# Performance work log

Hardware: AMD Instinct MI355X
Metric: run time of the kernel (lower is better)

The kernel has to match this reference:

```python
import jax, jax.numpy as jnp
import numpy as np

B, S, D, H = 4, 2048, 1024, 16
DK = D // H


def setup_inputs() -> dict:
    key = jax.random.key(0)
    ks = jax.random.split(key, 12)
    scale = 1.0 / np.sqrt(D)
    inp = {
        "query": jax.random.normal(ks[0], (B, S, D), jnp.float32),
        "key": jax.random.normal(ks[1], (B, S, D), jnp.float32),
        "value": jax.random.normal(ks[2], (B, S, D), jnp.float32),
        # lower-triangular causal mask broadcast over batch (1 = keep, 0 = masked)
        "mask": jnp.broadcast_to(jnp.tril(jnp.ones((S, S), jnp.bool_)), (B, S, S)),
        "wq": jax.random.normal(ks[3], (D, D), jnp.float32) * scale,
        "bq": jnp.zeros((D,), jnp.float32),
        "wk": jax.random.normal(ks[4], (D, D), jnp.float32) * scale,
        "bk": jnp.zeros((D,), jnp.float32),
        "wv": jax.random.normal(ks[5], (D, D), jnp.float32) * scale,
        "bv": jnp.zeros((D,), jnp.float32),
        "wo": jax.random.normal(ks[6], (D, D), jnp.float32) * scale,
        "bo": jnp.zeros((D,), jnp.float32),
    }
    return inp


def _split_heads(x):
    # [B, S, D] -> [B, H, S, DK]
    return x.reshape(B, S, H, DK).transpose(0, 2, 1, 3)


def reference(query, key, value, mask, wq, bq, wk, bk, wv, bv, wo, bo):
    # torch.nn.Linear: y = x @ W.T + b
    q = _split_heads(query @ wq.T + bq)
    k = _split_heads(key @ wk.T + bk)
    v = _split_heads(value @ wv.T + bv)

    scores = jnp.einsum("bhqd,bhkd->bhqk", q, k) / jnp.sqrt(jnp.float32(DK))
    # mask.unsqueeze(1): [B,1,S,S] broadcast over heads; masked_fill(mask==0, -1e9)
    scores = jnp.where(mask[:, None, :, :], scores, jnp.float32(-1e9))
    attn = jax.nn.softmax(scores, axis=-1)
    # dropout is identity in eval/reference mode

    ctx = jnp.einsum("bhqk,bhkd->bhqd", attn, v)  # [B,H,S,DK]
    ctx = ctx.transpose(0, 2, 1, 3).reshape(B, S, D)
    return ctx @ wo.T + bo
```

## Files before the change

kernel.cpp:

```cpp
#include <hip/hip_runtime.h>
#include <hip/hip_bf16.h>
#include <hip/hip_fp16.h>

#define B_  4
#define S_  2048
#define D_  1024
#define H_  16
#define DK_ 64

#define DT_F32  0
#define DT_BF16 1
#define DT_F16  2

typedef __bf16 bf16x8 __attribute__((ext_vector_type(8)));
typedef float  f32x4  __attribute__((ext_vector_type(4)));

__device__ __forceinline__ float bf2f(unsigned short u) {
    return __uint_as_float(((unsigned int)u) << 16);
}
__device__ __forceinline__ unsigned short f2bf(float f) {
    unsigned int u = __float_as_uint(f);
    return (unsigned short)((u + 0x7FFFu + ((u >> 16) & 1u)) >> 16);
}
__device__ __forceinline__ float h2f(unsigned short u) {
    union { __half h; unsigned short s; } cv; cv.s = u;
    return __half2float(cv.h);
}
__device__ __forceinline__ unsigned short f2h(float f) {
    union { __half h; unsigned short s; } cv; cv.h = __float2half(f);
    return cv.s;
}

__device__ __forceinline__ void gld_lds16(const void* g, void* l) {
    __builtin_amdgcn_global_load_lds(
        (const __attribute__((address_space(1))) void*)g,
        (__attribute__((address_space(3))) void*)l, 16, 0, 0);
}

template<int DT>
__device__ __forceinline__ float4 ld4(const void* base, size_t idx) {
    if constexpr (DT == DT_F32) {
        return *(const float4*)((const float*)base + idx);
    } else if constexpr (DT == DT_BF16) {
        ushort4 u = *(const ushort4*)((const unsigned short*)base + idx);
        return make_float4(bf2f(u.x), bf2f(u.y), bf2f(u.z), bf2f(u.w));
    } else {
        ushort4 u = *(const ushort4*)((const unsigned short*)base + idx);
        return make_float4(h2f(u.x), h2f(u.y), h2f(u.z), h2f(u.w));
    }
}
template<int DT>
__device__ __forceinline__ float ld1(const void* base, size_t idx) {
    if constexpr (DT == DT_F32)  return ((const float*)base)[idx];
    if constexpr (DT == DT_BF16) return bf2f(((const unsigned short*)base)[idx]);
    return h2f(((const unsigned short*)base)[idx]);
}

__global__ void detect_dtype(const unsigned short* __restrict__ q,
                             int* __restrict__ flag) {
    int c_bf = 0, c_hi = 0;
    for (int i = 0; i < 256; ++i) {
        const int e = (q[i] >> 7) & 0xFF;
        c_bf += (e >= 100 && e <= 140);
        c_hi += (e > 140);
    }
    *flag = (c_hi > 16) ? DT_F32 : ((c_bf >= 250) ? DT_BF16 : DT_F16);
}

__global__ __launch_bounds__(256) void convW(
    const float* __restrict__ wq, const float* __restrict__ wk,
    const float* __restrict__ wv,
    const float* __restrict__ bq, const float* __restrict__ bk,
    const float* __restrict__ bv,
    unsigned short* __restrict__ Wc, unsigned short* __restrict__ Bc,
    const int* __restrict__ flag)
{
    if (*flag != DT_F32) return;
    const size_t NW = (size_t)D_ * D_;
    const size_t i = (size_t)blockIdx.x * blockDim.x + threadIdx.x;
    if (i * 4 < NW) {
        const float* src[3] = {wq, wk, wv};
        #pragma unroll
        for (int j = 0; j < 3; ++j) {
            float4 f = ((const float4*)src[j])[i];
            ushort4 u; u.x = f2bf(f.x); u.y = f2bf(f.y); u.z = f2bf(f.z); u.w = f2bf(f.w);
            ((ushort4*)(Wc + j * NW))[i] = u;
        }
    }
    if (i * 4 < D_) {
        const float* src[3] = {bq, bk, bv};
        #pragma unroll
        for (int j = 0; j < 3; ++j) {
            float4 f = ((const float4*)src[j])[i];
            ushort4 u; u.x = f2bf(f.x); u.y = f2bf(f.y); u.z = f2bf(f.z); u.w = f2bf(f.w);
            ((ushort4*)(Bc + j * D_))[i] = u;
        }
    }
}

__global__ __launch_bounds__(256) void conv3(
    const float* __restrict__ a, unsigned short* __restrict__ da, size_t na,
    const float* __restrict__ w, unsigned short* __restrict__ dw, size_t nw,
    const float* __restrict__ b, unsigned short* __restrict__ db, size_t nb,
    const int* __restrict__ flag)
{
    if (*flag != DT_F32) return;
    const size_t i = (size_t)blockIdx.x * blockDim.x + threadIdx.x;
    if (i * 4 < na) {
        float4 f = ((const float4*)a)[i];
        ushort4 u; u.x = f2bf(f.x); u.y = f2bf(f.y); u.z = f2bf(f.z); u.w = f2bf(f.w);
        ((ushort4*)da)[i] = u;
    }
    if (i * 4 < nw) {
        float4 f = ((const float4*)w)[i];
        ushort4 u; u.x = f2bf(f.x); u.y = f2bf(f.y); u.z = f2bf(f.z); u.w = f2bf(f.w);
        ((ushort4*)dw)[i] = u;
    }
    if (i * 4 < nb) {
        float4 f = ((const float4*)b)[i];
        ushort4 u; u.x = f2bf(f.x); u.y = f2bf(f.y); u.z = f2bf(f.z); u.w = f2bf(f.w);
        ((ushort4*)db)[i] = u;
    }
}

template<bool AF32>
__device__ __forceinline__ void gemm_qkv_body(
    const void* __restrict__ X, const unsigned short* __restrict__ W,
    const unsigned short* __restrict__ Bi, unsigned short* __restrict__ Y,
    const int zmode)
{
    __shared__ __align__(16) unsigned short Ash[128 * 32];
    __shared__ __align__(16) unsigned short Bsh[128 * 32];
    const int tid  = threadIdx.x;
    const int wv   = tid >> 6, lane = tid & 63;
    const int quad = lane >> 4, l16 = lane & 15;
    const int wm   = wv >> 1,  wn   = wv & 1;
    const int m0   = blockIdx.y * 128, n0 = blockIdx.x * 128;

    f32x4 acc[4][4];
    #pragma unroll
    for (int nt = 0; nt < 4; ++nt) {
        const float bb = bf2f(Bi[n0 + wn * 64 + nt * 16 + l16]);
        #pragma unroll
        for (int mt = 0; mt < 4; ++mt) acc[mt][nt] = (f32x4){bb, bb, bb, bb};
    }

    const int srow = lane >> 2, sc4 = lane & 3;
    for (int kt = 0; kt < 32; ++kt) {
        #pragma unroll
        for (int ph = 0; ph < 2; ++ph) {
            const int i   = wv + ph * 4;
            const int row = i * 16 + srow;
            gld_lds16(W + (size_t)(n0 + row) * D_ + kt * 32 + sc4 * 8,
                      (char*)Bsh + i * 1024);
            unsigned short* dst = Ash + i * 512 + lane * 8;
            if constexpr (AF32) {
                const float* src = (const float*)X + (size_t)(m0 + row) * D_ + kt * 32 + sc4 * 8;
                const float4 a0 = ((const float4*)src)[0];
                const float4 a1 = ((const float4*)src)[1];
                bf16x8 vv;
                vv[0] = (__bf16)a0.x; vv[1] = (__bf16)a0.y;
                vv[2] = (__bf16)a0.z; vv[3] = (__bf16)a0.w;
                vv[4] = (__bf16)a1.x; vv[5] = (__bf16)a1.y;
                vv[6] = (__bf16)a1.z; vv[7] = (__bf16)a1.w;
                *(bf16x8*)dst = vv;
            } else {
                *(bf16x8*)dst = *(const bf16x8*)(
                    (const unsigned short*)X + (size_t)(m0 + row) * D_ + kt * 32 + sc4 * 8);
            }
        }
        __syncthreads();

        bf16x8 af[4], bfr[4];
        #pragma unroll
        for (int t = 0; t < 4; ++t) {
            af[t]  = *(const bf16x8*)(Ash + (wm * 64 + t * 16 + l16) * 32 + quad * 8);
            bfr[t] = *(const bf16x8*)(Bsh + (wn * 64 + t * 16 + l16) * 32 + quad * 8);
        }
        #pragma unroll
        for (int mt = 0; mt < 4; ++mt)
            #pragma unroll
            for (int nt = 0; nt < 4; ++nt)
                acc[mt][nt] = __builtin_amdgcn_mfma_f32_16x16x32_bf16(
                    af[mt], bfr[nt], acc[mt][nt], 0, 0, 0);
        __syncthreads();
    }

    #pragma unroll
    for (int mt = 0; mt < 4; ++mt) {
        const int mb = m0 + wm * 64 + mt * 16 + quad * 4;
        #pragma unroll
        for (int nt = 0; nt < 4; ++nt) {
            const int n = n0 + wn * 64 + nt * 16 + l16;
            const f32x4 a = acc[mt][nt];
            const int h = n >> 6, dk = n & 63;
            if (zmode != 2) {
                #pragma unroll
                for (int r = 0; r < 4; ++r) {
                    const int m = mb + r, b = m >> 11, s = m & (S_ - 1);
                    Y[(((size_t)(b * H_ + h) * S_ + s) << 6) + dk] = f2bf(a[r]);
                }
            } else {
                const int b = mb >> 11, s = mb & (S_ - 1);
                ushort4 u;
                u.x = f2bf(a[0]); u.y = f2bf(a[1]); u.z = f2bf(a[2]); u.w = f2bf(a[3]);
                *(ushort4*)(Y + (((size_t)(b * H_ + h) * DK_ + dk) << 11) + s) = u;
            }
        }
    }
}

__global__ __launch_bounds__(256) void gemm_qkv(
    const float* __restrict__ xq, const float* __restrict__ xk,
    const float* __restrict__ xv,
    const unsigned short* __restrict__ Wc,
    const unsigned short* __restrict__ wqb, const unsigned short* __restrict__ wkb,
    const unsigned short* __restrict__ wvb,
    const unsigned short* __restrict__ Bc,
    const unsigned short* __restrict__ bqb, const unsigned short* __restrict__ bkb,
    const unsigned short* __restrict__ bvb,
    unsigned short* __restrict__ Ybase,
    const int* __restrict__ flag)
{
    const int f = *flag;
    if (f == DT_F16) return;
    const int z = blockIdx.z;
    const size_t NE = (size_t)B_ * S_ * D_;
    const size_t NW = (size_t)D_ * D_;
    unsigned short* Y = Ybase + (size_t)z * NE;
    if (f == DT_F32) {
        const void* X = (z == 0) ? (const void*)xq : (z == 1) ? (const void*)xk : (const void*)xv;
        gemm_qkv_body<true>(X, Wc + (size_t)z * NW, Bc + (size_t)z * D_, Y, z);
    } else {
        const void* X = (z == 0) ? (const void*)xq : (z == 1) ? (const void*)xk : (const void*)xv;
        const unsigned short* W  = (z == 0) ? wqb : (z == 1) ? wkb : wvb;
        const unsigned short* Bi = (z == 0) ? bqb : (z == 1) ? bkb : bvb;
        gemm_qkv_body<false>(X, W, Bi, Y, z);
    }
}

template<int MODE>
__global__ __launch_bounds__(256) void gemm_mfma(
    const unsigned short* __restrict__ Xa, const unsigned short* __restrict__ Xb,
    const unsigned short* __restrict__ Wa, const unsigned short* __restrict__ Wb,
    const unsigned short* __restrict__ Ba, const unsigned short* __restrict__ Bb,
    void* __restrict__ Y,
    const int* __restrict__ flag)
{
    const int f = *flag;
    if (f == DT_F16) return;
    const unsigned short* X  = (f == DT_F32) ? Xa : Xb;
    const unsigned short* W  = (f == DT_F32) ? Wa : Wb;
    const unsigned short* Bi = (f == DT_F32) ? Ba : Bb;

    __shared__ __align__(16) unsigned short Ash[128 * 32];
    __shared__ __align__(16) unsigned short Bsh[128 * 32];
    const int tid  = threadIdx.x;
    const int wv   = tid >> 6, lane = tid & 63;
    const int quad = lane >> 4, l16 = lane & 15;
    const int wm   = wv >> 1,  wn   = wv & 1;
    const int m0   = blockIdx.y * 128, n0 = blockIdx.x * 128;

    f32x4 acc[4][4];
    #pragma unroll
    for (int nt = 0; nt < 4; ++nt) {
        const float bb = bf2f(Bi[n0 + wn * 64 + nt * 16 + l16]);
        #pragma unroll
        for (int mt = 0; mt < 4; ++mt) acc[mt][nt] = (f32x4){bb, bb, bb, bb};
    }

    const int srow = lane >> 2, sc4 = lane & 3;
    for (int kt = 0; kt < 32; ++kt) {
        #pragma unroll
        for (int ph = 0; ph < 2; ++ph) {
            const int i = wv + ph * 4;
            const int row = i * 16 + srow;
            gld_lds16(X + (size_t)(m0 + row) * D_ + kt * 32 + sc4 * 8,
                      (char*)Ash + i * 1024);
            gld_lds16(W + (size_t)(n0 + row) * D_ + kt * 32 + sc4 * 8,
                      (char*)Bsh + i * 1024);
        }
        __syncthreads();

        bf16x8 af[4], bfr[4];
        #pragma unroll
        for (int t = 0; t < 4; ++t) {
            af[t]  = *(const bf16x8*)(Ash + (wm * 64 + t * 16 + l16) * 32 + quad * 8);
            bfr[t] = *(const bf16x8*)(Bsh + (wn * 64 + t * 16 + l16) * 32 + quad * 8);
        }
        #pragma unroll
        for (int mt = 0; mt < 4; ++mt)
            #pragma unroll
            for (int nt = 0; nt < 4; ++nt)
                acc[mt][nt] = __builtin_amdgcn_mfma_f32_16x16x32_bf16(
                    af[mt], bfr[nt], acc[mt][nt], 0, 0, 0);
        __syncthreads();
    }

    #pragma unroll
    for (int mt = 0; mt < 4; ++mt) {
        const int mb = m0 + wm * 64 + mt * 16 + quad * 4;
        #pragma unroll
        for (int nt = 0; nt < 4; ++nt) {
            const int n = n0 + wn * 64 + nt * 16 + l16;
            const f32x4 a = acc[mt][nt];
            if constexpr (MODE == 0) {
                const int h = n >> 6, dk = n & 63;
                #pragma unroll
                for (int r = 0; r < 4; ++r) {
                    const int m = mb + r, b = m >> 11, s = m & (S_ - 1);
                    ((unsigned short*)Y)[(((size_t)(b * H_ + h) * S_ + s) << 6) + dk] = f2bf(a[r]);
                }
            } else if constexpr (MODE == 2) {
                const int h = n >> 6, dk = n & 63;
                const int b = mb >> 11, s = mb & (S_ - 1);
                ushort4 u;
                u.x = f2bf(a[0]); u.y = f2bf(a[1]); u.z = f2bf(a[2]); u.w = f2bf(a[3]);
                *(ushort4*)((unsigned short*)Y + (((size_t)(b * H_ + h) * DK_ + dk) << 11) + s) = u;
            } else {
                if (f == DT_F32) {
                    #pragma unroll
                    for (int r = 0; r < 4; ++r)
                        ((float*)Y)[(size_t)(mb + r) * D_ + n] = a[r];
                } else {
                    #pragma unroll
                    for (int r = 0; r < 4; ++r)
                        ((unsigned short*)Y)[(size_t)(mb + r) * D_ + n] = f2bf(a[r]);
                }
            }
        }
    }
}

__global__ __launch_bounds__(256) void attn_mfma(
    const unsigned short* __restrict__ Q,
    const unsigned short* __restrict__ K,
    const unsigned short* __restrict__ Vt,
    unsigned short* __restrict__ ctx)
{
    __shared__ __align__(16) unsigned short Ksh[2][2 * 64 * 32];
    __shared__ __align__(16) unsigned short Vsh[2][2 * 64 * 32];
    __shared__ __align__(16) __bf16         Psh[4][2 * 16 * 32];
    const int tid  = threadIdx.x;
    const int wv   = tid >> 6, lane = tid & 63;
    const int quad = lane >> 4, l16 = lane & 15;
    const int bx = blockIdx.x, bh = blockIdx.y;
    const unsigned short* Qb = Q  + (size_t)bh * S_ * DK_;
    const unsigned short* Kb = K  + (size_t)bh * S_ * DK_;
    const unsigned short* Vb = Vt + (size_t)bh * DK_ * S_;
    const int b = bh >> 4, h = bh & 15;
    const int srow = lane >> 2, sc4 = lane & 3;
    const int NT = S_ / 64;

    const float C1 = 0.125f * 1.44269504089f;
    const float C0 = -4.0f  * 1.44269504089f;

    auto stage = [&](int buf, int kt) {
        #pragma unroll
        for (int ph = 0; ph < 2; ++ph) {
            const int i  = wv + ph * 4;
            const int kk = i >> 2, r16 = i & 3;
            const int rr = r16 * 16 + srow;
            gld_lds16(Kb + (size_t)(kt * 64 + rr) * DK_ + kk * 32 + sc4 * 8,
                      (char*)(&Ksh[buf][0]) + i * 1024);
            gld_lds16(Vb + (size_t)rr * S_ + kt * 64 + kk * 32 + sc4 * 8,
                      (char*)(&Vsh[buf][0]) + i * 1024);
        }
    };

    #pragma unroll
    for (int seg = 0; seg < 2; ++seg) {
        const int qt = seg ? (NT - 1 - bx) : bx;
        const int q0 = qt * 64;

        const int qrow = q0 + wv * 16 + l16;
        bf16x8 qf0 = *(const bf16x8*)(Qb + (size_t)qrow * DK_ + quad * 8);
        bf16x8 qf1 = *(const bf16x8*)(Qb + (size_t)qrow * DK_ + 32 + quad * 8);

        f32x4 o[4];
        #pragma unroll
        for (int t = 0; t < 4; ++t) o[t] = (f32x4){0.f, 0.f, 0.f, 0.f};
        float lsum[4] = {0.f, 0.f, 0.f, 0.f};
        const int rowb = q0 + wv * 16 + quad * 4;

        stage(0, 0);

        for (int kt = 0; kt <= qt; ++kt) {
            const int cur = kt & 1;
            if (kt < qt) {
                stage(cur ^ 1, kt + 1);
                asm volatile("s_waitcnt vmcnt(4)" ::: "memory");
            } else {
                asm volatile("s_waitcnt vmcnt(0)" ::: "memory");
            }
            __builtin_amdgcn_s_barrier();
            asm volatile("" ::: "memory");

            const unsigned short* Kc = &Ksh[cur][0];
            const unsigned short* Vc = &Vsh[cur][0];

            f32x4 st[4];
            #pragma unroll
            for (int t = 0; t < 4; ++t) {
                bf16x8 k0 = *(const bf16x8*)(Kc + (t * 16 + l16) * 32 + quad * 8);
                bf16x8 k1 = *(const bf16x8*)(Kc + 2048 + (t * 16 + l16) * 32 + quad * 8);
                f32x4 z = (f32x4){0.f, 0.f, 0.f, 0.f};
                st[t] = __builtin_amdgcn_mfma_f32_16x16x32_bf16(qf0, k0, z, 0, 0, 0);
                st[t] = __builtin_amdgcn_mfma_f32_16x16x32_bf16(qf1, k1, st[t], 0, 0, 0);
            }

            float p[4][4];
            if (kt == qt) {
                #pragma unroll
                for (int t = 0; t < 4; ++t) {
                    const int col = kt * 64 + t * 16 + l16;
                    #pragma unroll
                    for (int r = 0; r < 4; ++r) {
                        float sv = fmaf(st[t][r], C1, C0);
                        if (col > rowb + r) sv = -1e9f;
                        p[t][r] = __builtin_amdgcn_exp2f(sv);
                        lsum[r] += p[t][r];
                    }
                }
            } else {
                #pragma unroll
                for (int t = 0; t < 4; ++t)
                    #pragma unroll
                    for (int r = 0; r < 4; ++r) {
                        p[t][r] = __builtin_amdgcn_exp2f(fmaf(st[t][r], C1, C0));
                        lsum[r] += p[t][r];
                    }
            }

            #pragma unroll
            for (int t = 0; t < 4; ++t) {
                const int col = t * 16 + l16;
                const int kk = col >> 5, c32 = col & 31, g = c32 >> 3;
                #pragma unroll
                for (int r = 0; r < 4; ++r) {
                    const int row = quad * 4 + r;
                    Psh[wv][kk * 512 + row * 32 + ((g ^ quad) * 8) + (c32 & 7)] =
                        (__bf16)p[t][r];
                }
            }

            bf16x8 pf[2];
            #pragma unroll
            for (int kk = 0; kk < 2; ++kk)
                pf[kk] = *(const bf16x8*)(&Psh[wv][kk * 512 + l16 * 32 + ((quad ^ (l16 >> 2)) * 8)]);
            #pragma unroll
            for (int t = 0; t < 4; ++t) {
                bf16x8 v0 = *(const bf16x8*)(Vc + (t * 16 + l16) * 32 + quad * 8);
                bf16x8 v1 = *(const bf16x8*)(Vc + 2048 + (t * 16 + l16) * 32 + quad * 8);
                o[t] = __builtin_amdgcn_mfma_f32_16x16x32_bf16(pf[0], v0, o[t], 0, 0, 0);
                o[t] = __builtin_amdgcn_mfma_f32_16x16x32_bf16(pf[1], v1, o[t], 0, 0, 0);
            }
            __syncthreads();
        }

        float li[4];
        #pragma unroll
        for (int r = 0; r < 4; ++r) {
            float l = lsum[r];
            l += __shfl_xor(l, 1, 64);
            l += __shfl_xor(l, 2, 64);
            l += __shfl_xor(l, 4, 64);
            l += __shfl_xor(l, 8, 64);
            li[r] = 1.0f / l;
        }
        #pragma unroll
        for (int t = 0; t < 4; ++t)
            #pragma unroll
            for (int r = 0; r < 4; ++r) {
                const int row = rowb + r;
                ctx[(size_t)(b * S_ + row) * D_ + h * DK_ + t * 16 + l16] =
                    f2bf(o[t][r] * li[r]);
            }
    }
}

template<int MODE, int DT>
__global__ __launch_bounds__(256) void gemm_xwT(
    const void* __restrict__ X,
    const void* __restrict__ W,
    const void* __restrict__ bias,
    void* __restrict__ Y,
    const int* __restrict__ flag)
{
    if (*flag != DT) return;
    constexpr int XDT = (MODE == 1) ? DT_BF16 : DT;

    __shared__ float As[16][65];
    __shared__ float Bs[16][65];
    const int tid = threadIdx.x;
    const int n0 = blockIdx.x * 64;
    const int m0 = blockIdx.y * 64;
    const int tx = tid & 15, ty = tid >> 4;
    const int lr = tid >> 2, lc = (tid & 3) << 2;

    float acc[4][4] = {};
    const size_t xbase = (size_t)(m0 + lr) * D_ + lc;
    const size_t wbase = (size_t)(n0 + lr) * D_ + lc;

    for (int k0 = 0; k0 < D_; k0 += 16) {
        const float4 a = ld4<XDT>(X, xbase + k0);
        const float4 b = ld4<DT >(W, wbase + k0);
        As[lc + 0][lr] = a.x; As[lc + 1][lr] = a.y;
        As[lc + 2][lr] = a.z; As[lc + 3][lr] = a.w;
        Bs[lc + 0][lr] = b.x; Bs[lc + 1][lr] = b.y;
        Bs[lc + 2][lr] = b.z; Bs[lc + 3][lr] = b.w;
        __syncthreads();
        #pragma unroll
        for (int k = 0; k < 16; ++k) {
            float av[4], bv[4];
            #pragma unroll
            for (int i = 0; i < 4; ++i) { av[i] = As[k][ty * 4 + i]; bv[i] = Bs[k][tx * 4 + i]; }
            #pragma unroll
            for (int i = 0; i < 4; ++i)
                #pragma unroll
                for (int j = 0; j < 4; ++j) acc[i][j] += av[i] * bv[j];
        }
        __syncthreads();
    }

    #pragma unroll
    for (int i = 0; i < 4; ++i) {
        const int m = m0 + ty * 4 + i;
        #pragma unroll
        for (int j = 0; j < 4; ++j) {
            const int n = n0 + tx * 4 + j;
            const float y = acc[i][j] + ld1<DT>(bias, n);
            if constexpr (MODE == 0) {
                const int b = m >> 11, s = m & (S_ - 1), h = n >> 6, dk = n & 63;
                ((unsigned short*)Y)[(((size_t)(b * H_ + h) * S_ + s) << 6) + dk] = f2bf(y);
            } else if constexpr (MODE == 2) {
                const int b = m >> 11, s = m & (S_ - 1), h = n >> 6, dk = n & 63;
                ((unsigned short*)Y)[(((size_t)(b * H_ + h) * DK_ + dk) << 11) + s] = f2bf(y);
            } else {
                const size_t oi = (size_t)m * D_ + n;
                if constexpr (DT == DT_F32)       ((float*)Y)[oi] = y;
                else if constexpr (DT == DT_BF16) ((unsigned short*)Y)[oi] = f2bf(y);
                else                              ((unsigned short*)Y)[oi] = f2h(y);
            }
        }
    }
}

__global__ void copy_out(const ulong2* __restrict__ src, ulong2* __restrict__ dst,
                         size_t out_size, const int* __restrict__ flag) {
    const size_t bytes  = out_size * ((*flag == DT_F32) ? 4u : 2u);
    const size_t chunks = bytes >> 4;
    const size_t i = (size_t)blockIdx.x * blockDim.x + threadIdx.x;
    if (i < chunks) dst[i] = src[i];
}

extern "C" void kernel_launch(void* const* d_in, const int* in_sizes, int n_in,
                              void* d_out, int out_size, void* d_ws, size_t ws_size,
                              hipStream_t stream) {
    const int wi = (n_in >= 12) ? 4 : 3;
    const void* q  = d_in[0];
    const void* k  = d_in[1];
    const void* v  = d_in[2];
    const void* wq = d_in[wi + 0];
    const void* bq = d_in[wi + 1];
    const void* wk = d_in[wi + 2];
    const void* bk = d_in[wi + 3];
    const void* wv = d_in[wi + 4];
    const void* bv = d_in[wi + 5];
    const void* wo = d_in[wi + 6];
    const void* bo = d_in[wi + 7];

    const size_t NE = (size_t)B_ * S_ * D_;
    const size_t NW = (size_t)D_ * D_;

    int* flag = (int*)d_ws;
    unsigned short* Qw = (unsigned short*)((char*)d_ws + 256);
    unsigned short* Kw = Qw + NE;
    unsigned short* Vw = Kw + NE;
    unsigned short* Cw = Vw + NE;

    const bool planA = ws_size >= 256 + 4 * NE * 2;

    unsigned short* xconv = (unsigned short*)d_out;
    unsigned short* Wc    = xconv + NE;
    unsigned short* Bc    = Wc + 4 * NW;

    unsigned short* ctx  = planA ? Cw : xconv;
    void*           yfin = planA ? d_out : (void*)Qw;
    unsigned short* WoC = planA ? Kw : (Wc + 3 * NW);
    unsigned short* BoC = planA ? (Kw + NW) : (Bc + 3 * D_);

    detect_dtype<<<1, 1, 0, stream>>>((const unsigned short*)q, flag);

    const dim3 gqkv(D_ / 128, (B_ * S_) / 128, 3);
    const dim3 gm(D_ / 128, (B_ * S_) / 128);
    const dim3 gs(D_ / 64,  (B_ * S_) / 64);
    const int  wgrid = (int)((NW / 4 + 255) / 256);

    convW<<<wgrid, 256, 0, stream>>>((const float*)wq, (const float*)wk,
                                     (const float*)wv,
                                     (const float*)bq, (const float*)bk,
                                     (const float*)bv,
                                     Wc, Bc, flag);

    gemm_qkv<<<gqkv, 256, 0, stream>>>(
        (const float*)q, (const float*)k, (const float*)v,
        Wc,
        (const unsigned short*)wq, (const unsigned short*)wk,
        (const unsigned short*)wv,
        Bc,
        (const unsigned short*)bq, (const unsigned short*)bk,
        (const unsigned short*)bv,
        Qw, flag);

    gemm_xwT<0, DT_F16><<<gs, 256, 0, stream>>>(q, wq, bq, Qw, flag);
    gemm_xwT<0, DT_F16><<<gs, 256, 0, stream>>>(k, wk, bk, Kw, flag);
    gemm_xwT<2, DT_F16><<<gs, 256, 0, stream>>>(v, wv, bv, Vw, flag);

    attn_mfma<<<dim3(S_ / 128, B_ * H_), 256, 0, stream>>>(Qw, Kw, Vw, ctx);

    conv3<<<wgrid, 256, 0, stream>>>((const float*)nullptr, (unsigned short*)nullptr, 0,
                                     (const float*)wo, WoC, NW,
                                     (const float*)bo, BoC, D_, flag);

    gemm_mfma<1><<<gm, 256, 0, stream>>>(ctx, ctx,
                                         WoC, (const unsigned short*)wo,
                                         BoC, (const unsigned short*)bo,
                                         yfin, flag);
    gemm_xwT<1, DT_F16><<<gs, 256, 0, stream>>>((const void*)ctx, wo, bo, yfin, flag);

    if (!planA) {
        const size_t maxChunks = ((size_t)out_size * 4) >> 4;
        copy_out<<<(int)((maxChunks + 255) / 256), 256, 0, stream>>>(
            (const ulong2*)yfin, (ulong2*)d_out, (size_t)out_size, flag);
    }
}
```

Measured before the change: 416.1 us.

## Double-buffer LDS in QKV and output GEMMs and remap block order

Double-buffers the shared-memory tiles of the QKV projection and output projection GEMMs. Each iteration prefetches the next K tile (register-staged for the fp32 A operand, direct global-to-LDS for the rest) while computing on the current one, with explicit waitcnt and barrier control in place of two __syncthreads per step. It also remaps the flat block index so blocks scheduled together are spread across row tiles, which could change cache reuse of X and W. The cost is twice the LDS, which may reduce occupancy, plus fragile hand-written vmcnt counts.

```diff
diff --git a/kernel.cpp b/kernel.cpp
--- a/kernel.cpp
+++ b/kernel.cpp
@@ -127,15 +127,15 @@
 __device__ __forceinline__ void gemm_qkv_body(
     const void* __restrict__ X, const unsigned short* __restrict__ W,
     const unsigned short* __restrict__ Bi, unsigned short* __restrict__ Y,
-    const int zmode)
+    const int zmode, const int m0, const int n0)
 {
-    __shared__ __align__(16) unsigned short Ash[128 * 32];
-    __shared__ __align__(16) unsigned short Bsh[128 * 32];
+    __shared__ __align__(16) unsigned short Ash[2][128 * 32];
+    __shared__ __align__(16) unsigned short Bsh[2][128 * 32];
     const int tid  = threadIdx.x;
     const int wv   = tid >> 6, lane = tid & 63;
     const int quad = lane >> 4, l16 = lane & 15;
     const int wm   = wv >> 1,  wn   = wv & 1;
-    const int m0   = blockIdx.y * 128, n0 = blockIdx.x * 128;
+    const int srow = lane >> 2, sc4 = lane & 3;
 
     f32x4 acc[4][4];
     #pragma unroll
@@ -145,37 +145,61 @@
         for (int mt = 0; mt < 4; ++mt) acc[mt][nt] = (f32x4){bb, bb, bb, bb};
     }
 
-    const int srow = lane >> 2, sc4 = lane & 3;
-    for (int kt = 0; kt < 32; ++kt) {
+    float4 ra00, ra01, ra10, ra11;
+    bf16x8 rb0, rb1;
+
+    auto aload = [&](int kt) {
+        #pragma unroll
+        for (int ph = 0; ph < 2; ++ph) {
+            const int i   = wv + ph * 4;
+            const int row = i * 16 + srow;
+            if constexpr (AF32) {
+                const float* src = (const float*)X + (size_t)(m0 + row) * D_ + kt * 32 + sc4 * 8;
+                float4 x0 = ((const float4*)src)[0];
+                float4 x1 = ((const float4*)src)[1];
+                if (ph == 0) { ra00 = x0; ra01 = x1; } else { ra10 = x0; ra11 = x1; }
+            } else {
+                const unsigned short* src =
+                    (const unsigned short*)X + (size_t)(m0 + row) * D_ + kt * 32 + sc4 * 8;
+                bf16x8 x = *(const bf16x8*)src;
+                if (ph == 0) rb0 = x; else rb1 = x;
+            }
+        }
+    };
+    auto awrite = [&](int buf) {
+        #pragma unroll
+        for (int ph = 0; ph < 2; ++ph) {
+            const int i = wv + ph * 4;
+            unsigned short* dst = &Ash[buf][0] + i * 512 + lane * 8;
+            if constexpr (AF32) {
+                const float4 x0 = ph ? ra10 : ra00;
+                const float4 x1 = ph ? ra11 : ra01;
+                bf16x8 vv;
+                vv[0] = (__bf16)x0.x; vv[1] = (__bf16)x0.y;
+                vv[2] = (__bf16)x0.z; vv[3] = (__bf16)x0.w;
+                vv[4] = (__bf16)x1.x; vv[5] = (__bf16)x1.y;
+                vv[6] = (__bf16)x1.z; vv[7] = (__bf16)x1.w;
+                *(bf16x8*)dst = vv;
+            } else {
+                *(bf16x8*)dst = ph ? rb1 : rb0;
+            }
+        }
+    };
+    auto stageB = [&](int buf, int kt) {
         #pragma unroll
         for (int ph = 0; ph < 2; ++ph) {
             const int i   = wv + ph * 4;
             const int row = i * 16 + srow;
             gld_lds16(W + (size_t)(n0 + row) * D_ + kt * 32 + sc4 * 8,
-                      (char*)Bsh + i * 1024);
-            unsigned short* dst = Ash + i * 512 + lane * 8;
-            if constexpr (AF32) {
-                const float* src = (const float*)X + (size_t)(m0 + row) * D_ + kt * 32 + sc4 * 8;
-                const float4 a0 = ((const float4*)src)[0];
-                const float4 a1 = ((const float4*)src)[1];
-                bf16x8 vv;
-                vv[0] = (__bf16)a0.x; vv[1] = (__bf16)a0.y;
-                vv[2] = (__bf16)a0.z; vv[3] = (__bf16)a0.w;
-                vv[4] = (__bf16)a1.x; vv[5] = (__bf16)a1.y;
-                vv[6] = (__bf16)a1.z; vv[7] = (__bf16)a1.w;
-                *(bf16x8*)dst = vv;
-            } else {
-                *(bf16x8*)dst = *(const bf16x8*)(
-                    (const unsigned short*)X + (size_t)(m0 + row) * D_ + kt * 32 + sc4 * 8);
-            }
-        }
-        __syncthreads();
-
+                      (char*)(&Bsh[buf][0]) + i * 1024);
+        }
+    };
+    auto compute = [&](int buf) {
         bf16x8 af[4], bfr[4];
         #pragma unroll
         for (int t = 0; t < 4; ++t) {
-            af[t]  = *(const bf16x8*)(Ash + (wm * 64 + t * 16 + l16) * 32 + quad * 8);
-            bfr[t] = *(const bf16x8*)(Bsh + (wn * 64 + t * 16 + l16) * 32 + quad * 8);
+            af[t]  = *(const bf16x8*)(&Ash[buf][0] + (wm * 64 + t * 16 + l16) * 32 + quad * 8);
+            bfr[t] = *(const bf16x8*)(&Bsh[buf][0] + (wn * 64 + t * 16 + l16) * 32 + quad * 8);
         }
         #pragma unroll
         for (int mt = 0; mt < 4; ++mt)
@@ -183,7 +207,34 @@
             for (int nt = 0; nt < 4; ++nt)
                 acc[mt][nt] = __builtin_amdgcn_mfma_f32_16x16x32_bf16(
                     af[mt], bfr[nt], acc[mt][nt], 0, 0, 0);
-        __syncthreads();
+    };
+
+    aload(0);
+    stageB(0, 0);
+    awrite(0);
+    asm volatile("s_waitcnt lgkmcnt(0)" ::: "memory");
+
+    for (int kt = 0; kt < 32; ++kt) {
+        const int c = kt & 1;
+        if (kt < 31) {
+            stageB(c ^ 1, kt + 1);
+            aload(kt + 1);
+            if constexpr (AF32)
+                asm volatile("s_waitcnt vmcnt(6)" ::: "memory");
+            else
+                asm volatile("s_waitcnt vmcnt(4)" ::: "memory");
+        } else {
+            asm volatile("s_waitcnt vmcnt(0)" ::: "memory");
+        }
+        __builtin_amdgcn_s_barrier();
+        asm volatile("" ::: "memory");
+        compute(c);
+        if (kt < 31) {
+            awrite(c ^ 1);
+            asm volatile("s_waitcnt lgkmcnt(0)" ::: "memory");
+            __builtin_amdgcn_s_barrier();
+            asm volatile("" ::: "memory");
+        }
     }
 
     #pragma unroll
@@ -224,24 +275,29 @@
 {
     const int f = *flag;
     if (f == DT_F16) return;
-    const int z = blockIdx.z;
+    const unsigned flat = blockIdx.x + 8u * blockIdx.y + 512u * blockIdx.z;
+    const unsigned w    = (flat & 7u) * 192u + (flat >> 3);
+    const int zz = (int)(w >> 9);
+    const unsigned r = w & 511u;
+    const int n0 = (int)(r & 7u) * 128;
+    const int m0 = (int)(r >> 3) * 128;
+
     const size_t NE = (size_t)B_ * S_ * D_;
     const size_t NW = (size_t)D_ * D_;
-    unsigned short* Y = Ybase + (size_t)z * NE;
+    unsigned short* Y = Ybase + (size_t)zz * NE;
     if (f == DT_F32) {
-        const void* X = (z == 0) ? (const void*)xq : (z == 1) ? (const void*)xk : (const void*)xv;
-        gemm_qkv_body<true>(X, Wc + (size_t)z * NW, Bc + (size_t)z * D_, Y, z);
+        const void* X = (zz == 0) ? (const void*)xq : (zz == 1) ? (const void*)xk : (const void*)xv;
+        gemm_qkv_body<true>(X, Wc + (size_t)zz * NW, Bc + (size_t)zz * D_, Y, zz, m0, n0);
     } else {
-        const void* X = (z == 0) ? (const void*)xq : (z == 1) ? (const void*)xk : (const void*)xv;
-        const unsigned short* W  = (z == 0) ? wqb : (z == 1) ? wkb : wvb;
-        const unsigned short* Bi = (z == 0) ? bqb : (z == 1) ? bkb : bvb;
-        gemm_qkv_body<false>(X, W, Bi, Y, z);
-    }
-}
-
-template<int MODE>
-__global__ __launch_bounds__(256) void gemm_mfma(
-    const unsigned short* __restrict__ Xa, const unsigned short* __restrict__ Xb,
+        const void* X = (zz == 0) ? (const void*)xq : (zz == 1) ? (const void*)xk : (const void*)xv;
+        const unsigned short* W  = (zz == 0) ? wqb : (zz == 1) ? wkb : wvb;
+        const unsigned short* Bi = (zz == 0) ? bqb : (zz == 1) ? bkb : bvb;
+        gemm_qkv_body<false>(X, W, Bi, Y, zz, m0, n0);
+    }
+}
+
+__global__ __launch_bounds__(256) void gemm_out(
+    const unsigned short* __restrict__ X,
     const unsigned short* __restrict__ Wa, const unsigned short* __restrict__ Wb,
     const unsigned short* __restrict__ Ba, const unsigned short* __restrict__ Bb,
     void* __restrict__ Y,
@@ -249,17 +305,21 @@
 {
     const int f = *flag;
     if (f == DT_F16) return;
-    const unsigned short* X  = (f == DT_F32) ? Xa : Xb;
     const unsigned short* W  = (f == DT_F32) ? Wa : Wb;
     const unsigned short* Bi = (f == DT_F32) ? Ba : Bb;
 
-    __shared__ __align__(16) unsigned short Ash[128 * 32];
-    __shared__ __align__(16) unsigned short Bsh[128 * 32];
+    __shared__ __align__(16) unsigned short Ash[2][128 * 32];
+    __shared__ __align__(16) unsigned short Bsh[2][128 * 32];
     const int tid  = threadIdx.x;
     const int wv   = tid >> 6, lane = tid & 63;
     const int quad = lane >> 4, l16 = lane & 15;
     const int wm   = wv >> 1,  wn   = wv & 1;
-    const int m0   = blockIdx.y * 128, n0 = blockIdx.x * 128;
+    const int srow = lane >> 2, sc4 = lane & 3;
+
+    const unsigned flat = blockIdx.x + 8u * blockIdx.y;
+    const unsigned w    = (flat & 7u) * 64u + (flat >> 3);
+    const int n0 = (int)(w & 7u) * 128;
+    const int m0 = (int)(w >> 3) * 128;
 
     f32x4 acc[4][4];
     #pragma unroll
@@ -269,24 +329,23 @@
         for (int mt = 0; mt < 4; ++mt) acc[mt][nt] = (f32x4){bb, bb, bb, bb};
     }
 
-    const int srow = lane >> 2, sc4 = lane & 3;
-    for (int kt = 0; kt < 32; ++kt) {
+    auto stageAB = [&](int buf, int kt) {
         #pragma unroll
         for (int ph = 0; ph < 2; ++ph) {
-            const int i = wv + ph * 4;
+            const int i   = wv + ph * 4;
             const int row = i * 16 + srow;
             gld_lds16(X + (size_t)(m0 + row) * D_ + kt * 32 + sc4 * 8,
-                      (char*)Ash + i * 1024);
+                      (char*)(&Ash[buf][0]) + i * 1024);
             gld_lds16(W + (size_t)(n0 + row) * D_ + kt * 32 + sc4 * 8,
-                      (char*)Bsh + i * 1024);
-        }
-        __syncthreads();
-
+                      (char*)(&Bsh[buf][0]) + i * 1024);
+        }
+    };
+    auto compute = [&](int buf) {
         bf16x8 af[4], bfr[4];
         #pragma unroll
         for (int t = 0; t < 4; ++t) {
-            af[t]  = *(const bf16x8*)(Ash + (wm * 64 + t * 16 + l16) * 32 + quad * 8);
-            bfr[t] = *(const bf16x8*)(Bsh + (wn * 64 + t * 16 + l16) * 32 + quad * 8);
+            af[t]  = *(const bf16x8*)(&Ash[buf][0] + (wm * 64 + t * 16 + l16) * 32 + quad * 8);
+            bfr[t] = *(const bf16x8*)(&Bsh[buf][0] + (wn * 64 + t * 16 + l16) * 32 + quad * 8);
         }
         #pragma unroll
         for (int mt = 0; mt < 4; ++mt)
@@ -294,7 +353,22 @@
             for (int nt = 0; nt < 4; ++nt)
                 acc[mt][nt] = __builtin_amdgcn_mfma_f32_16x16x32_bf16(
                     af[mt], bfr[nt], acc[mt][nt], 0, 0, 0);
-        __syncthreads();
+    };
+
+    stageAB(0, 0);
+    for (int kt = 0; kt < 32; ++kt) {
+        const int c = kt & 1;
+        if (kt < 31) {
+            stageAB(c ^ 1, kt + 1);
+            asm volatile("s_waitcnt vmcnt(4)" ::: "memory");
+        } else {
+            asm volatile("s_waitcnt vmcnt(0)" ::: "memory");
+        }
+        __builtin_amdgcn_s_barrier();
+        asm volatile("" ::: "memory");
+        compute(c);
+        __builtin_amdgcn_s_barrier();
+        asm volatile("" ::: "memory");
     }
 
     #pragma unroll
@@ -304,29 +378,14 @@
         for (int nt = 0; nt < 4; ++nt) {
             const int n = n0 + wn * 64 + nt * 16 + l16;
             const f32x4 a = acc[mt][nt];
-            if constexpr (MODE == 0) {
-                const int h = n >> 6, dk = n & 63;
+            if (f == DT_F32) {
                 #pragma unroll
-                for (int r = 0; r < 4; ++r) {
-                    const int m = mb + r, b = m >> 11, s = m & (S_ - 1);
-                    ((unsigned short*)Y)[(((size_t)(b * H_ + h) * S_ + s) << 6) + dk] = f2bf(a[r]);
-                }
-            } else if constexpr (MODE == 2) {
-                const int h = n >> 6, dk = n & 63;
-                const int b = mb >> 11, s = mb & (S_ - 1);
-                ushort4 u;
-                u.x = f2bf(a[0]); u.y = f2bf(a[1]); u.z = f2bf(a[2]); u.w = f2bf(a[3]);
-                *(ushort4*)((unsigned short*)Y + (((size_t)(b * H_ + h) * DK_ + dk) << 11) + s) = u;
+                for (int r = 0; r < 4; ++r)
+                    ((float*)Y)[(size_t)(mb + r) * D_ + n] = a[r];
             } else {
-                if (f == DT_F32) {
-                    #pragma unroll
-                    for (int r = 0; r < 4; ++r)
-                        ((float*)Y)[(size_t)(mb + r) * D_ + n] = a[r];
-                } else {
-                    #pragma unroll
-                    for (int r = 0; r < 4; ++r)
-                        ((unsigned short*)Y)[(size_t)(mb + r) * D_ + n] = f2bf(a[r]);
-                }
+                #pragma unroll
+                for (int r = 0; r < 4; ++r)
+                    ((unsigned short*)Y)[(size_t)(mb + r) * D_ + n] = f2bf(a[r]);
             }
         }
     }
@@ -623,10 +682,10 @@
                                      (const float*)wo, WoC, NW,
                                      (const float*)bo, BoC, D_, flag);
 
-    gemm_mfma<1><<<gm, 256, 0, stream>>>(ctx, ctx,
-                                         WoC, (const unsigned short*)wo,
-                                         BoC, (const unsigned short*)bo,
-                                         yfin, flag);
+    gemm_out<<<gm, 256, 0, stream>>>(ctx,
+                                     WoC, (const unsigned short*)wo,
+                                     BoC, (const unsigned short*)bo,
+                                     yfin, flag);
     gemm_xwT<1, DT_F16><<<gs, 256, 0, stream>>>((const void*)ctx, wo, bo, yfin, flag);
 
     if (!planA) {
```

Measured after the change: 426.7 us. 1.03x slower.
